# Optimization experiments

Hardware: AMD Instinct MI355X
Metric: run time of the kernel (lower is better)

## Reference

```python
import jax, jax.numpy as jnp
import numpy as np
from jax import lax

B = 8192
NUM_EXPERTS = 5
TOP_K = 3
NUM_CLASSES = 10
FEAT = 5 * 5 * 64  # 1600, flatten dim after conv stack on 28x28x1


def _conv(x, w, b):
    # NHWC input, HWIO kernel, VALID padding, stride 1
    y = lax.conv_general_dilated(x, w, (1, 1), 'VALID',
                                 dimension_numbers=('NHWC', 'HWIO', 'NHWC'))
    return y + b


def _maxpool2(x):
    return lax.reduce_window(x, -jnp.inf, lax.max,
                             (1, 2, 2, 1), (1, 2, 2, 1), 'VALID')


def setup_inputs() -> dict:
    key = jax.random.key(0)
    ks = jax.random.split(key, 8)
    x = jax.random.normal(ks[0], (B, 28, 28, 1), dtype=jnp.float32)
    # conv kernels: glorot-ish small init
    conv1_w = jax.random.normal(ks[1], (3, 3, 1, 32), dtype=jnp.float32) * 0.1
    conv1_b = jnp.zeros((32,), jnp.float32)
    conv2_w = jax.random.normal(ks[2], (3, 3, 32, 64), dtype=jnp.float32) * 0.05
    conv2_b = jnp.zeros((64,), jnp.float32)
    # gating + experts use RandomNormal(stddev=0.001), zero bias per source
    gate_w = jax.random.normal(ks[3], (FEAT, NUM_EXPERTS), dtype=jnp.float32) * 0.001
    gate_b = jnp.zeros((NUM_EXPERTS,), jnp.float32)
    exp_w = jax.random.normal(ks[4], (NUM_EXPERTS, FEAT, NUM_CLASSES), dtype=jnp.float32) * 0.001
    exp_b = jnp.zeros((NUM_EXPERTS, NUM_CLASSES), jnp.float32)
    return {'x': x, 'conv1_w': conv1_w, 'conv1_b': conv1_b,
            'conv2_w': conv2_w, 'conv2_b': conv2_b,
            'gate_w': gate_w, 'gate_b': gate_b,
            'exp_w': exp_w, 'exp_b': exp_b}


def reference(x, conv1_w, conv1_b, conv2_w, conv2_b, gate_w, gate_b, exp_w, exp_b):
    # conv backbone (dropout is identity at inference)
    h = jax.nn.relu(_conv(x, conv1_w, conv1_b))        # [B,26,26,32]
    h = _maxpool2(h)                                   # [B,13,13,32]
    h = jax.nn.relu(_conv(h, conv2_w, conv2_b))        # [B,11,11,64]
    h = _maxpool2(h)                                   # [B,5,5,64]
    feat = h.reshape(h.shape[0], -1)                   # [B,1600]

    # gating: softmax over experts, then top-k
    gates = jax.nn.softmax(feat @ gate_w + gate_b)     # [B,E]
    top_w, top_idx = lax.top_k(gates, TOP_K)           # [B,K], [B,K]

    # all-expert outputs (E small), gather the selected ones, weighted combine
    all_out = jnp.einsum('bd,edh->beh', feat, exp_w) + exp_b   # [B,E,C]
    top_out = jnp.take_along_axis(all_out, top_idx[:, :, None], axis=1)  # [B,K,C]
    combined = jnp.einsum('bkh,bk->bh', top_out, top_w)        # [B,C]

    return jax.nn.softmax(combined)
```

## Files before the change

### kernel.cpp

```cpp
#include <hip/hip_runtime.h>
#include <hip/hip_bf16.h>

#define BLOCK 512
#define IPB 8
#define EIPB 16
#define FB_STRIDE 1616
#define ES_STRIDE 1608
#define H1_STRIDE 40

#define W2T_OFF 0
#define EWT_OFF 18432
#define W1C_OFF 120832
#define WS_SHORTS 121856
#define FEAT_OFF 121856

typedef __attribute__((ext_vector_type(8))) short short8;
typedef __attribute__((ext_vector_type(4))) float f32x4;

#define SEL_LO 0x05040100u

static __device__ __forceinline__ unsigned short f2bf(float f) {
    unsigned int u = __builtin_bit_cast(unsigned int, f);
    u = (u + 0x7FFFu + ((u >> 16) & 1u)) >> 16;
    return (unsigned short)u;
}
static __device__ __forceinline__ float bf2f(unsigned short h) {
    unsigned int u = ((unsigned int)h) << 16;
    return __builtin_bit_cast(float, u);
}
static __device__ __forceinline__ unsigned int cvtpk(float a, float b) {
    unsigned int r;
    asm("v_cvt_pk_bf16_f32 %0, %1, %2" : "=v"(r) : "v"(a), "v"(b));
    return r;
}

__global__ void moe_prep(const float* __restrict__ w2, const float* __restrict__ gw,
                         const float* __restrict__ ew, const float* __restrict__ w1,
                         unsigned short* __restrict__ ws) {
    int i = blockIdx.x * 256 + threadIdx.x;
    if (i < 18432) {
        int kpos = i >> 11, rem = i & 2047, oc = rem >> 5, j = rem & 31;
        int ic = ((j & 1) << 4) | (j >> 1);
        ws[W2T_OFF + i] = f2bf(w2[(kpos * 32 + ic) * 64 + oc]);
    }
    int j2 = i - EWT_OFF;
    if (j2 >= 0 && j2 < 102400) {
        int ks = j2 >> 11, rem = j2 & 2047, n = rem >> 5, k = rem & 31;
        int kk = ks * 32 + k;
        int wv = kk >> 6, jj = kk & 63;
        int r = jj & 31;
        int oc = ((jj >> 5) << 5) | ((r & 1) << 4) | (r >> 1);
        int d = wv * 64 + oc;
        float v = 0.f;
        if (n < 50)      v = ew[(n / 10) * 16000 + d * 10 + (n % 10)];
        else if (n < 55) v = gw[d * 5 + (n - 50)];
        ws[EWT_OFF + j2] = f2bf(v);
    }
    int p = i - W1C_OFF;
    if (p >= 0 && p < 1024) {
        int n = p >> 5, k = p & 31;
        unsigned short val = 0;
        if (k < 9) {
            val = f2bf(w1[k * 32 + n]);
        } else if (k >= 16 && k < 25) {
            float w = w1[(k - 16) * 32 + n];
            unsigned short hi = f2bf(w);
            val = f2bf(w - bf2f(hi));
        }
        ws[W1C_OFF + p] = val;
    }
}

__global__ __launch_bounds__(BLOCK, 3)
void moe_conv(const float* __restrict__ x, const float* __restrict__ b1,
              const float* __restrict__ b2, const unsigned short* __restrict__ ws,
              unsigned short* __restrict__ feat, int B)
{
    __shared__ unsigned int xsp[2][784];
    __shared__ __align__(16) unsigned short h1p[2][169 * H1_STRIDE];

    const int tid  = threadIdx.x;
    const int wid  = tid >> 6;
    const int lane = tid & 63;
    const int l15  = lane & 15;
    const int lg   = lane >> 4;

    const int mt0 = wid >> 1;
    const int n0  = (wid & 1) * 2;
    short8 bfA[9], bfB[9];
    #pragma unroll
    for (int kp = 0; kp < 9; kp++) {
        bfA[kp] = *(const short8*)&ws[W2T_OFF + (kp * 64 + n0 * 16 + l15) * 32 + lg * 8];
        bfB[kp] = *(const short8*)&ws[W2T_OFF + (kp * 64 + (n0 + 1) * 16 + l15) * 32 + lg * 8];
    }
    const short8 c1f0 = *(const short8*)&ws[W1C_OFF + l15 * 32 + lg * 8];
    const short8 c1f1 = *(const short8*)&ws[W1C_OFF + (16 + l15) * 32 + lg * 8];

    const float bias1a = b1[l15];
    const float bias1b = b1[16 + l15];
    const float bias2a = b2[n0 * 16 + l15];
    const float bias2b = b2[n0 * 16 + l15 + 16];

    int xoff1[6], hoff1[6];
    bool val1[6];
    #pragma unroll
    for (int j = 0; j < 6; ++j) {
        const int mt = wid + 8 * j;
        int wsrc = mt * 4 + (l15 >> 2); if (wsrc > 168) wsrc = 168;
        const int s = l15 & 3;
        const int cy = 2 * (wsrc / 13) + (s >> 1);
        const int cx = 2 * (wsrc % 13) + (s & 1);
        xoff1[j] = cy * 28 + cx;
        const int window = mt * 4 + lg;
        val1[j] = (mt < 43) && (window < 169);
        hoff1[j] = (window < 169 ? window : 0) * H1_STRIDE + 2 * l15;
    }
    int aoff2[2], foff2[2];
    bool val2[2];
    #pragma unroll
    for (int mi = 0; mi < 2; ++mi) {
        const int mt = mt0 + mi * 4;
        const int m = mt * 16 + l15;
        int wsrc = m >> 2; if (wsrc > 24) wsrc = 24;
        const int s = m & 3;
        const int cy = 2 * (wsrc / 5) + (s >> 1);
        const int cx = 2 * (wsrc % 5) + (s & 1);
        aoff2[mi] = (cy * 13 + cx) * (H1_STRIDE * 2) + lg * 16;
        const int wv = mt * 4 + lg;
        val2[mi] = (wv < 25);
        foff2[mi] = (wv < 25 ? wv : 0) * 64 + ((n0 >> 1) << 5) + 2 * l15;
    }

    const int img0 = blockIdx.x * IPB;
    {
        int im = img0 < B ? img0 : B - 1;
        const float* xg = x + (size_t)im * 784;
        xsp[0][tid] = cvtpk(xg[tid], xg[tid]);
        if (tid + BLOCK < 784) xsp[0][tid + BLOCK] = cvtpk(xg[tid + BLOCK], xg[tid + BLOCK]);
    }
    __syncthreads();

    #pragma unroll
    for (int p = 0; p <= IPB; ++p) {
        const bool do_c1 = (p < IPB);
        const bool do_c2 = (p >= 1);
        const bool pre   = (p + 1 < IPB);

        float f0 = 0.f, f1 = 0.f;
        if (pre) {
            int im2 = img0 + p + 1; if (im2 >= B) im2 = B - 1;
            const float* xg2 = x + (size_t)im2 * 784;
            f0 = xg2[tid];
            if (tid + BLOCK < 784) f1 = xg2[tid + BLOCK];
        }

        if (do_c2) {
            const int it = p - 1;
            const int img = img0 + it;
            const unsigned short* h1cur = h1p[it & 1];
            unsigned short* frow = feat + (size_t)img * 1600;
            #pragma unroll
            for (int mi = 0; mi < 2; ++mi) {
                const char* abase = (const char*)h1cur + aoff2[mi];
                f32x4 a0 = {0.f, 0.f, 0.f, 0.f};
                f32x4 a1 = {0.f, 0.f, 0.f, 0.f};
                #pragma unroll
                for (int kp = 0; kp < 9; kp++) {
                    const int ky = kp / 3, kx = kp % 3;
                    const short8 af = *(const short8*)(abase + (ky * 13 + kx) * (H1_STRIDE * 2));
                    a0 = __builtin_amdgcn_mfma_f32_16x16x32_bf16(af, bfA[kp], a0, 0, 0, 0);
                    a1 = __builtin_amdgcn_mfma_f32_16x16x32_bf16(af, bfB[kp], a1, 0, 0, 0);
                }
                if (val2[mi] && img < B) {
                    const float m0 = fmaxf(fmaxf(a0.x, a0.y), fmaxf(a0.z, a0.w)) + bias2a;
                    const float m1 = fmaxf(fmaxf(a1.x, a1.y), fmaxf(a1.z, a1.w)) + bias2b;
                    *(unsigned int*)&frow[foff2[mi]] = cvtpk(fmaxf(m0, 0.f), fmaxf(m1, 0.f));
                }
            }
        }

        if (do_c1) {
            const unsigned int* xcur = xsp[p & 1];
            unsigned short* h1dst = h1p[p & 1];
            #pragma unroll
            for (int j = 0; j < 6; ++j) {
                if (wid + 8 * j < 43) {
                    const unsigned int* xb = xcur + xoff1[j];
                    unsigned int a0 = 0u, a1 = 0u, a2 = 0u, a3 = 0u;
                    if ((lg & 1) == 0) {
                        const unsigned int t0 = xb[0],  t1 = xb[1],  t2 = xb[2];
                        const unsigned int t3 = xb[28], t4 = xb[29], t5 = xb[30];
                        const unsigned int t6 = xb[56], t7 = xb[57];
                        a0 = __builtin_amdgcn_perm(t1, t0, SEL_LO);
                        a1 = __builtin_amdgcn_perm(t3, t2, SEL_LO);
                        a2 = __builtin_amdgcn_perm(t5, t4, SEL_LO);
                        a3 = __builtin_amdgcn_perm(t7, t6, SEL_LO);
                    } else {
                        a0 = xb[58] & 0xffffu;
                    }
                    const uint4 av = make_uint4(a0, a1, a2, a3);
                    const short8 af = __builtin_bit_cast(short8, av);
                    f32x4 p0 = {0.f, 0.f, 0.f, 0.f};
                    f32x4 p1 = {0.f, 0.f, 0.f, 0.f};
                    p0 = __builtin_amdgcn_mfma_f32_16x16x32_bf16(af, c1f0, p0, 0, 0, 0);
                    p1 = __builtin_amdgcn_mfma_f32_16x16x32_bf16(af, c1f1, p1, 0, 0, 0);
                    if (val1[j]) {
                        const float m0 = fmaxf(fmaxf(p0.x, p0.y), fmaxf(p0.z, p0.w)) + bias1a;
                        const float m1 = fmaxf(fmaxf(p1.x, p1.y), fmaxf(p1.z, p1.w)) + bias1b;
                        *(unsigned int*)&h1dst[hoff1[j]] = cvtpk(fmaxf(m0, 0.f), fmaxf(m1, 0.f));
                    }
                }
            }
        }

        if (pre) {
            xsp[(p + 1) & 1][tid] = cvtpk(f0, f0);
            if (tid + BLOCK < 784) xsp[(p + 1) & 1][tid + BLOCK] = cvtpk(f1, f1);
        }
        __syncthreads();
    }
}

__global__ __launch_bounds__(BLOCK, 2)
void moe_expert(const unsigned short* __restrict__ ws, const float* __restrict__ gb,
                const float* __restrict__ eb, float* __restrict__ out, int B)
{
    __shared__ __align__(16) unsigned short featS[EIPB * ES_STRIDE];
    __shared__ float allC[2][EIPB][64];

    const int tid  = threadIdx.x;
    const int wid  = tid >> 6;
    const int lane = tid & 63;
    const int l15  = lane & 15;
    const int lg   = lane >> 4;

    const unsigned short* feat = ws + FEAT_OFF;
    const unsigned short* ewt  = ws + EWT_OFF;
    const int img0 = blockIdx.x * EIPB;

    for (int i = tid; i < EIPB * 800; i += BLOCK) {
        const int r = i / 800, c = i - r * 800;
        const int img = img0 + r;
        unsigned int v = 0u;
        if (img < B) v = *(const unsigned int*)&feat[(size_t)img * 1600 + 2 * c];
        *(unsigned int*)&featS[r * ES_STRIDE + 2 * c] = v;
    }
    __syncthreads();

    {
        const int kh  = wid >> 2;
        const int ntE = wid & 3;
        const int bc  = ntE * 16 + l15;
        f32x4 acc = {0.f, 0.f, 0.f, 0.f};
        const int ks0 = kh * 25;
        for (int ks = ks0; ks < ks0 + 25; ++ks) {
            const short8 af = *(const short8*)&featS[l15 * ES_STRIDE + ks * 32 + lg * 8];
            const short8 bf = *(const short8*)&ewt[(ks * 64 + bc) * 32 + lg * 8];
            acc = __builtin_amdgcn_mfma_f32_16x16x32_bf16(af, bf, acc, 0, 0, 0);
        }
        const int r0 = lg * 4;
        allC[kh][r0 + 0][bc] = acc.x;
        allC[kh][r0 + 1][bc] = acc.y;
        allC[kh][r0 + 2][bc] = acc.z;
        allC[kh][r0 + 3][bc] = acc.w;
    }
    __syncthreads();

    if (tid < EIPB) {
        const int img = img0 + tid;
        if (img < B) {
            float gv[5], mx = -1e30f;
            #pragma unroll
            for (int g = 0; g < 5; g++) {
                gv[g] = allC[0][tid][50 + g] + allC[1][tid][50 + g] + gb[g];
                mx = fmaxf(mx, gv[g]);
            }
            float ssum = 0.f;
            #pragma unroll
            for (int g = 0; g < 5; g++) { gv[g] = expf(gv[g] - mx); ssum += gv[g]; }
            const float inv = 1.f / ssum;
            #pragma unroll
            for (int g = 0; g < 5; g++) gv[g] *= inv;

            int idx0, idx1, idx2; float wv0, wv1, wv2;
            unsigned usedMask = 0;
            {
                int bi = 0; float bv = -1e30f;
                #pragma unroll
                for (int g = 0; g < 5; g++)
                    if (gv[g] > bv) { bv = gv[g]; bi = g; }
                idx0 = bi; wv0 = bv; usedMask |= (1u << bi);
            }
            {
                int bi = 0; float bv = -1e30f;
                #pragma unroll
                for (int g = 0; g < 5; g++)
                    if (!(usedMask & (1u << g)) && gv[g] > bv) { bv = gv[g]; bi = g; }
                idx1 = bi; wv1 = bv; usedMask |= (1u << bi);
            }
            {
                int bi = 0; float bv = -1e30f;
                #pragma unroll
                for (int g = 0; g < 5; g++)
                    if (!(usedMask & (1u << g)) && gv[g] > bv) { bv = gv[g]; bi = g; }
                idx2 = bi; wv2 = bv;
            }
            float comb[10];
            #pragma unroll
            for (int cc = 0; cc < 10; cc++) {
                comb[cc] = wv0 * (allC[0][tid][idx0 * 10 + cc] + allC[1][tid][idx0 * 10 + cc] + eb[idx0 * 10 + cc])
                         + wv1 * (allC[0][tid][idx1 * 10 + cc] + allC[1][tid][idx1 * 10 + cc] + eb[idx1 * 10 + cc])
                         + wv2 * (allC[0][tid][idx2 * 10 + cc] + allC[1][tid][idx2 * 10 + cc] + eb[idx2 * 10 + cc]);
            }
            float m2 = -1e30f;
            #pragma unroll
            for (int cc = 0; cc < 10; cc++) m2 = fmaxf(m2, comb[cc]);
            float e[10], s2 = 0.f;
            #pragma unroll
            for (int cc = 0; cc < 10; cc++) { e[cc] = expf(comb[cc] - m2); s2 += e[cc]; }
            const float inv2 = 1.f / s2;
            #pragma unroll
            for (int cc = 0; cc < 10; cc++) out[(size_t)img * 10 + cc] = e[cc] * inv2;
        }
    }
}

__global__ __launch_bounds__(BLOCK, 3)
void moe_main_fused(const float* __restrict__ x, const float* __restrict__ b1,
                    const float* __restrict__ b2, const float* __restrict__ gb,
                    const float* __restrict__ eb, const unsigned short* __restrict__ ws,
                    float* __restrict__ out, int B)
{
    __shared__ unsigned int xsp[2][784];
    __shared__ __align__(16) unsigned short h1p[2][169 * H1_STRIDE];
    __shared__ __align__(16) unsigned short featbuf[4 * FB_STRIDE];
    __shared__ float allC[2][4 * 56];

    const int tid  = threadIdx.x;
    const int wid  = tid >> 6;
    const int lane = tid & 63;
    const int l15  = lane & 15;
    const int lg   = lane >> 4;

    const int mt0 = wid >> 1;
    const int n0  = (wid & 1) * 2;
    short8 bfA[9], bfB[9];
    #pragma unroll
    for (int kp = 0; kp < 9; kp++) {
        bfA[kp] = *(const short8*)&ws[W2T_OFF + (kp * 64 + n0 * 16 + l15) * 32 + lg * 8];
        bfB[kp] = *(const short8*)&ws[W2T_OFF + (kp * 64 + (n0 + 1) * 16 + l15) * 32 + lg * 8];
    }
    const short8 c1f0 = *(const short8*)&ws[W1C_OFF + l15 * 32 + lg * 8];
    const short8 c1f1 = *(const short8*)&ws[W1C_OFF + (16 + l15) * 32 + lg * 8];

    const float bias1a = b1[l15];
    const float bias1b = b1[16 + l15];
    const float bias2a = b2[n0 * 16 + l15];
    const float bias2b = b2[n0 * 16 + l15 + 16];

    const int img0 = blockIdx.x * 4;
    {
        int im = img0 < B ? img0 : B - 1;
        const float* xg = x + (size_t)im * 784;
        xsp[0][tid] = cvtpk(xg[tid], xg[tid]);
        if (tid + BLOCK < 784) xsp[0][tid + BLOCK] = cvtpk(xg[tid + BLOCK], xg[tid + BLOCK]);
    }
    __syncthreads();

    #pragma unroll
    for (int p = 0; p <= 4; ++p) {
        const bool do_c1 = (p < 4);
        const bool do_c2 = (p >= 1);
        const bool pre   = (p + 1 < 4);

        float f0 = 0.f, f1 = 0.f;
        if (pre) {
            int im2 = img0 + p + 1; if (im2 >= B) im2 = B - 1;
            const float* xg2 = x + (size_t)im2 * 784;
            f0 = xg2[tid];
            if (tid + BLOCK < 784) f1 = xg2[tid + BLOCK];
        }

        if (do_c2) {
            const int it = p - 1;
            const unsigned short* h1cur = h1p[it & 1];
            #pragma unroll
            for (int mi = 0; mi < 2; ++mi) {
                const int mt = mt0 + mi * 4;
                const int m = mt * 16 + l15;
                int wsrc = m >> 2; if (wsrc > 24) wsrc = 24;
                const int s = m & 3;
                const int cy = 2 * (wsrc / 5) + (s >> 1);
                const int cx = 2 * (wsrc % 5) + (s & 1);
                const char* abase = (const char*)h1cur + (cy * 13 + cx) * (H1_STRIDE * 2) + lg * 16;
                f32x4 a0 = {0.f, 0.f, 0.f, 0.f};
                f32x4 a1 = {0.f, 0.f, 0.f, 0.f};
                #pragma unroll
                for (int kp = 0; kp < 9; kp++) {
                    const int ky = kp / 3, kx = kp % 3;
                    const short8 af = *(const short8*)(abase + (ky * 13 + kx) * (H1_STRIDE * 2));
                    a0 = __builtin_amdgcn_mfma_f32_16x16x32_bf16(af, bfA[kp], a0, 0, 0, 0);
                    a1 = __builtin_amdgcn_mfma_f32_16x16x32_bf16(af, bfB[kp], a1, 0, 0, 0);
                }
                const int wv = mt * 4 + lg;
                if (wv < 25) {
                    const float m0 = fmaxf(fmaxf(a0.x, a0.y), fmaxf(a0.z, a0.w)) + bias2a;
                    const float m1 = fmaxf(fmaxf(a1.x, a1.y), fmaxf(a1.z, a1.w)) + bias2b;
                    *(unsigned int*)&featbuf[it * FB_STRIDE + wv * 64 + ((n0 >> 1) << 5) + 2 * l15] =
                        cvtpk(fmaxf(m0, 0.f), fmaxf(m1, 0.f));
                }
            }
        }

        if (do_c1) {
            const unsigned int* xcur = xsp[p & 1];
            unsigned short* h1dst = h1p[p & 1];
            for (int mt = wid; mt < 43; mt += 8) {
                int wsrc = mt * 4 + (l15 >> 2); if (wsrc > 168) wsrc = 168;
                const int s  = l15 & 3;
                const int cy = 2 * (wsrc / 13) + (s >> 1);
                const int cx = 2 * (wsrc % 13) + (s & 1);
                const unsigned int* xb = &xcur[cy * 28 + cx];
                unsigned int a0 = 0u, a1 = 0u, a2 = 0u, a3 = 0u;
                if ((lg & 1) == 0) {
                    const unsigned int t0 = xb[0],  t1 = xb[1],  t2 = xb[2];
                    const unsigned int t3 = xb[28], t4 = xb[29], t5 = xb[30];
                    const unsigned int t6 = xb[56], t7 = xb[57];
                    a0 = __builtin_amdgcn_perm(t1, t0, SEL_LO);
                    a1 = __builtin_amdgcn_perm(t3, t2, SEL_LO);
                    a2 = __builtin_amdgcn_perm(t5, t4, SEL_LO);
                    a3 = __builtin_amdgcn_perm(t7, t6, SEL_LO);
                } else {
                    a0 = xb[58] & 0xffffu;
                }
                const uint4 av = make_uint4(a0, a1, a2, a3);
                const short8 af = __builtin_bit_cast(short8, av);
                f32x4 p0 = {0.f, 0.f, 0.f, 0.f};
                f32x4 p1 = {0.f, 0.f, 0.f, 0.f};
                p0 = __builtin_amdgcn_mfma_f32_16x16x32_bf16(af, c1f0, p0, 0, 0, 0);
                p1 = __builtin_amdgcn_mfma_f32_16x16x32_bf16(af, c1f1, p1, 0, 0, 0);
                const int window = mt * 4 + lg;
                if (window < 169) {
                    const float m0 = fmaxf(fmaxf(p0.x, p0.y), fmaxf(p0.z, p0.w)) + bias1a;
                    const float m1 = fmaxf(fmaxf(p1.x, p1.y), fmaxf(p1.z, p1.w)) + bias1b;
                    *(unsigned int*)&h1dst[window * H1_STRIDE + 2 * l15] =
                        cvtpk(fmaxf(m0, 0.f), fmaxf(m1, 0.f));
                }
            }
        }

        if (pre) {
            xsp[(p + 1) & 1][tid] = cvtpk(f0, f0);
            if (tid + BLOCK < 784) xsp[(p + 1) & 1][tid + BLOCK] = cvtpk(f1, f1);
        }
        __syncthreads();
    }

    {
        const unsigned short* ewt = ws + EWT_OFF;
        const int kh = wid >> 2;
        const int ntE = wid & 3;
        const int bc = ntE * 16 + l15;
        const int arow = l15 & 3;
        f32x4 acc = {0.f, 0.f, 0.f, 0.f};
        const int ks0 = kh * 25;
        for (int ks = ks0; ks < ks0 + 25; ++ks) {
            const short8 af = *(const short8*)&featbuf[arow * FB_STRIDE + ks * 32 + lg * 8];
            const short8 bf = *(const short8*)&ewt[(ks * 64 + bc) * 32 + lg * 8];
            acc = __builtin_amdgcn_mfma_f32_16x16x32_bf16(af, bf, acc, 0, 0, 0);
        }
        if (lane < 16 && bc < 56) {
            allC[kh][0 * 56 + bc] = acc.x;
            allC[kh][1 * 56 + bc] = acc.y;
            allC[kh][2 * 56 + bc] = acc.z;
            allC[kh][3 * 56 + bc] = acc.w;
        }
    }
    __syncthreads();

    if (tid < 4) {
        const int img = img0 + tid;
        if (img < B) {
            float gv[5], mx = -1e30f;
            #pragma unroll
            for (int g = 0; g < 5; g++) {
                gv[g] = allC[0][tid * 56 + 50 + g] + allC[1][tid * 56 + 50 + g] + gb[g];
                mx = fmaxf(mx, gv[g]);
            }
            float ssum = 0.f;
            #pragma unroll
            for (int g = 0; g < 5; g++) { gv[g] = expf(gv[g] - mx); ssum += gv[g]; }
            const float inv = 1.f / ssum;
            #pragma unroll
            for (int g = 0; g < 5; g++) gv[g] *= inv;

            int idx0, idx1, idx2; float wv0, wv1, wv2;
            unsigned usedMask = 0;
            {
                int bi = 0; float bv = -1e30f;
                #pragma unroll
                for (int g = 0; g < 5; g++)
                    if (gv[g] > bv) { bv = gv[g]; bi = g; }
                idx0 = bi; wv0 = bv; usedMask |= (1u << bi);
            }
            {
                int bi = 0; float bv = -1e30f;
                #pragma unroll
                for (int g = 0; g < 5; g++)
                    if (!(usedMask & (1u << g)) && gv[g] > bv) { bv = gv[g]; bi = g; }
                idx1 = bi; wv1 = bv; usedMask |= (1u << bi);
            }
            {
                int bi = 0; float bv = -1e30f;
                #pragma unroll
                for (int g = 0; g < 5; g++)
                    if (!(usedMask & (1u << g)) && gv[g] > bv) { bv = gv[g]; bi = g; }
                idx2 = bi; wv2 = bv;
            }
            float comb[10];
            #pragma unroll
            for (int cc = 0; cc < 10; cc++) {
                comb[cc] = wv0 * (allC[0][tid * 56 + idx0 * 10 + cc] + allC[1][tid * 56 + idx0 * 10 + cc] + eb[idx0 * 10 + cc])
                         + wv1 * (allC[0][tid * 56 + idx1 * 10 + cc] + allC[1][tid * 56 + idx1 * 10 + cc] + eb[idx1 * 10 + cc])
                         + wv2 * (allC[0][tid * 56 + idx2 * 10 + cc] + allC[1][tid * 56 + idx2 * 10 + cc] + eb[idx2 * 10 + cc]);
            }
            float m2 = -1e30f;
            #pragma unroll
            for (int cc = 0; cc < 10; cc++) m2 = fmaxf(m2, comb[cc]);
            float e[10], s2 = 0.f;
            #pragma unroll
            for (int cc = 0; cc < 10; cc++) { e[cc] = expf(comb[cc] - m2); s2 += e[cc]; }
            const float inv2 = 1.f / s2;
            #pragma unroll
            for (int cc = 0; cc < 10; cc++) out[(size_t)img * 10 + cc] = e[cc] * inv2;
        }
    }
}

extern "C" void kernel_launch(void* const* d_in, const int* in_sizes, int n_in,
                              void* d_out, int out_size, void* d_ws, size_t ws_size,
                              hipStream_t stream) {
    const float* x   = (const float*)d_in[0];
    const float* w1  = (const float*)d_in[1];
    const float* b1  = (const float*)d_in[2];
    const float* w2  = (const float*)d_in[3];
    const float* b2  = (const float*)d_in[4];
    const float* gw  = (const float*)d_in[5];
    const float* gb  = (const float*)d_in[6];
    const float* ew  = (const float*)d_in[7];
    const float* eb  = (const float*)d_in[8];
    float* out = (float*)d_out;
    const int B = in_sizes[0] / 784;

    unsigned short* ws = (unsigned short*)d_ws;
    const size_t ws_full = ((size_t)WS_SHORTS + (size_t)B * 1600) * sizeof(unsigned short);

    moe_prep<<<(WS_SHORTS + 255) / 256, 256, 0, stream>>>(w2, gw, ew, w1, ws);
    if (ws_size >= ws_full) {
        moe_conv<<<(B + IPB - 1) / IPB, BLOCK, 0, stream>>>(x, b1, b2, ws, ws + FEAT_OFF, B);
        moe_expert<<<(B + EIPB - 1) / EIPB, BLOCK, 0, stream>>>(ws, gb, eb, out, B);
    } else {
        moe_main_fused<<<(B + 3) / 4, BLOCK, 0, stream>>>(x, b1, b2, gb, eb, ws, out, B);
    }
}
```

Before: 80.26 us.

## Stream conv2 weights from global memory per MFMA and raise occupancy to four blocks

Conv2 weight fragments are no longer held in 36 short8 registers per thread. They are now loaded from global memory (L1/L2-resident workspace) inside the MFMA loop. Each wave now covers one M-tile across all four N-tiles instead of two M-tiles across two N-tiles. The freed registers allow launch bounds of four blocks per CU instead of three. The cost is repeated global weight loads every image iteration, which may add latency and cache traffic that offsets the occupancy gain.

Result: slower. 256.6 us (+219.7%).

```diff
diff --git a/kernel.cpp b/kernel.cpp
--- a/kernel.cpp
+++ b/kernel.cpp
@@ -71,7 +71,7 @@
     }
 }
 
-__global__ __launch_bounds__(BLOCK, 3)
+__global__ __launch_bounds__(BLOCK, 4)
 void moe_conv(const float* __restrict__ x, const float* __restrict__ b1,
               const float* __restrict__ b2, const unsigned short* __restrict__ ws,
               unsigned short* __restrict__ feat, int B)
@@ -85,21 +85,15 @@
     const int l15  = lane & 15;
     const int lg   = lane >> 4;
 
-    const int mt0 = wid >> 1;
-    const int n0  = (wid & 1) * 2;
-    short8 bfA[9], bfB[9];
-    #pragma unroll
-    for (int kp = 0; kp < 9; kp++) {
-        bfA[kp] = *(const short8*)&ws[W2T_OFF + (kp * 64 + n0 * 16 + l15) * 32 + lg * 8];
-        bfB[kp] = *(const short8*)&ws[W2T_OFF + (kp * 64 + (n0 + 1) * 16 + l15) * 32 + lg * 8];
-    }
     const short8 c1f0 = *(const short8*)&ws[W1C_OFF + l15 * 32 + lg * 8];
     const short8 c1f1 = *(const short8*)&ws[W1C_OFF + (16 + l15) * 32 + lg * 8];
 
     const float bias1a = b1[l15];
     const float bias1b = b1[16 + l15];
-    const float bias2a = b2[n0 * 16 + l15];
-    const float bias2b = b2[n0 * 16 + l15 + 16];
+    const float bias2v0 = b2[l15];
+    const float bias2v1 = b2[16 + l15];
+    const float bias2v2 = b2[32 + l15];
+    const float bias2v3 = b2[48 + l15];
 
     int xoff1[6], hoff1[6];
     bool val1[6];
@@ -115,21 +109,24 @@
         val1[j] = (mt < 43) && (window < 169);
         hoff1[j] = (window < 169 ? window : 0) * H1_STRIDE + 2 * l15;
     }
-    int aoff2[2], foff2[2];
-    bool val2[2];
-    #pragma unroll
-    for (int mi = 0; mi < 2; ++mi) {
-        const int mt = mt0 + mi * 4;
+    int aoff2, foff2;
+    bool val2;
+    {
+        const int mt = wid;
         const int m = mt * 16 + l15;
         int wsrc = m >> 2; if (wsrc > 24) wsrc = 24;
         const int s = m & 3;
         const int cy = 2 * (wsrc / 5) + (s >> 1);
         const int cx = 2 * (wsrc % 5) + (s & 1);
-        aoff2[mi] = (cy * 13 + cx) * (H1_STRIDE * 2) + lg * 16;
+        aoff2 = (cy * 13 + cx) * (H1_STRIDE * 2) + lg * 16;
         const int wv = mt * 4 + lg;
-        val2[mi] = (wv < 25);
-        foff2[mi] = (wv < 25 ? wv : 0) * 64 + ((n0 >> 1) << 5) + 2 * l15;
-    }
+        val2 = (wv < 25);
+        foff2 = (wv < 25 ? wv : 0) * 64 + 2 * l15;
+    }
+    const unsigned short* bf0 = ws + W2T_OFF + (0 * 16 + l15) * 32 + lg * 8;
+    const unsigned short* bf1 = ws + W2T_OFF + (1 * 16 + l15) * 32 + lg * 8;
+    const unsigned short* bf2p = ws + W2T_OFF + (2 * 16 + l15) * 32 + lg * 8;
+    const unsigned short* bf3 = ws + W2T_OFF + (3 * 16 + l15) * 32 + lg * 8;
 
     const int img0 = blockIdx.x * IPB;
     {
@@ -159,23 +156,27 @@
             const int img = img0 + it;
             const unsigned short* h1cur = h1p[it & 1];
             unsigned short* frow = feat + (size_t)img * 1600;
-            #pragma unroll
-            for (int mi = 0; mi < 2; ++mi) {
-                const char* abase = (const char*)h1cur + aoff2[mi];
-                f32x4 a0 = {0.f, 0.f, 0.f, 0.f};
-                f32x4 a1 = {0.f, 0.f, 0.f, 0.f};
-                #pragma unroll
-                for (int kp = 0; kp < 9; kp++) {
-                    const int ky = kp / 3, kx = kp % 3;
-                    const short8 af = *(const short8*)(abase + (ky * 13 + kx) * (H1_STRIDE * 2));
-                    a0 = __builtin_amdgcn_mfma_f32_16x16x32_bf16(af, bfA[kp], a0, 0, 0, 0);
-                    a1 = __builtin_amdgcn_mfma_f32_16x16x32_bf16(af, bfB[kp], a1, 0, 0, 0);
-                }
-                if (val2[mi] && img < B) {
-                    const float m0 = fmaxf(fmaxf(a0.x, a0.y), fmaxf(a0.z, a0.w)) + bias2a;
-                    const float m1 = fmaxf(fmaxf(a1.x, a1.y), fmaxf(a1.z, a1.w)) + bias2b;
-                    *(unsigned int*)&frow[foff2[mi]] = cvtpk(fmaxf(m0, 0.f), fmaxf(m1, 0.f));
-                }
+            const char* abase = (const char*)h1cur + aoff2;
+            f32x4 a0 = {0.f, 0.f, 0.f, 0.f};
+            f32x4 a1 = {0.f, 0.f, 0.f, 0.f};
+            f32x4 a2 = {0.f, 0.f, 0.f, 0.f};
+            f32x4 a3 = {0.f, 0.f, 0.f, 0.f};
+            #pragma unroll
+            for (int kp = 0; kp < 9; kp++) {
+                const int ky = kp / 3, kx = kp % 3;
+                const short8 af = *(const short8*)(abase + (ky * 13 + kx) * (H1_STRIDE * 2));
+                a0 = __builtin_amdgcn_mfma_f32_16x16x32_bf16(af, *(const short8*)(bf0 + kp * 2048), a0, 0, 0, 0);
+                a1 = __builtin_amdgcn_mfma_f32_16x16x32_bf16(af, *(const short8*)(bf1 + kp * 2048), a1, 0, 0, 0);
+                a2 = __builtin_amdgcn_mfma_f32_16x16x32_bf16(af, *(const short8*)(bf2p + kp * 2048), a2, 0, 0, 0);
+                a3 = __builtin_amdgcn_mfma_f32_16x16x32_bf16(af, *(const short8*)(bf3 + kp * 2048), a3, 0, 0, 0);
+            }
+            if (val2 && img < B) {
+                const float m0 = fmaxf(fmaxf(a0.x, a0.y), fmaxf(a0.z, a0.w)) + bias2v0;
+                const float m1 = fmaxf(fmaxf(a1.x, a1.y), fmaxf(a1.z, a1.w)) + bias2v1;
+                const float m2 = fmaxf(fmaxf(a2.x, a2.y), fmaxf(a2.z, a2.w)) + bias2v2;
+                const float m3 = fmaxf(fmaxf(a3.x, a3.y), fmaxf(a3.z, a3.w)) + bias2v3;
+                *(unsigned int*)&frow[foff2]      = cvtpk(fmaxf(m0, 0.f), fmaxf(m1, 0.f));
+                *(unsigned int*)&frow[foff2 + 32] = cvtpk(fmaxf(m2, 0.f), fmaxf(m3, 0.f));
             }
         }
 
```
